# Performance work log

Measured on AMD Instinct MI355X. Metric: run time of the kernel, lower is better.

## Reference

```python
import jax, jax.numpy as jnp
import numpy as np

D_MODEL = 1024
N_HEADS = 16
HEAD_DIM = D_MODEL // N_HEADS
EPS = 1e-5


def _rope_tables(T, dim, dtype):
    inv_freq = 1.0 / (10000.0 ** (np.arange(0, dim, 2, dtype=np.float32) / dim))
    t = np.arange(T, dtype=np.float32)
    freqs = np.einsum('i,j->ij', t, inv_freq)            # [T, dim/2]
    emb = np.concatenate([freqs, freqs], axis=-1)        # [T, dim]
    return jnp.asarray(np.cos(emb), dtype), jnp.asarray(np.sin(emb), dtype)


def _rotate(x, cos, sin):
    # x: [B, T, H, hd]; cos/sin: [T, hd] broadcast over B, H
    c = cos[None, :, None, :]
    s = sin[None, :, None, :]
    x1, x2 = jnp.split(x, 2, axis=-1)
    return x * c + jnp.concatenate([-x2, x1], axis=-1) * s


def setup_inputs() -> dict:
    key = jax.random.key(0)
    k1, k2, k3 = jax.random.split(key, 3)
    B, T = 2, 2048
    x = jax.random.normal(k1, (B, T, D_MODEL), jnp.float32)
    norm_w = jnp.ones((D_MODEL,), jnp.float32)
    w_qkv = jax.random.normal(k2, (D_MODEL, 3 * D_MODEL), jnp.float32) * (D_MODEL ** -0.5)
    w_out = jax.random.normal(k3, (D_MODEL, D_MODEL), jnp.float32) * (D_MODEL ** -0.5)
    return {"x": x, "norm_w": norm_w, "w_qkv": w_qkv, "w_out": w_out}


def reference(x, norm_w, w_qkv, w_out):
    B, T, D = x.shape
    residual = x
    # RMSNorm
    h = x * jax.lax.rsqrt(jnp.mean(x * x, axis=-1, keepdims=True) + EPS) * norm_w
    # QKV projection
    qkv = (h @ w_qkv).reshape(B, T, 3, N_HEADS, HEAD_DIM)
    q, k, v = qkv[:, :, 0], qkv[:, :, 1], qkv[:, :, 2]   # [B, T, H, hd]
    # RoPE
    cos, sin = _rope_tables(T, HEAD_DIM, x.dtype)
    q = _rotate(q, cos, sin)
    k = _rotate(k, cos, sin)
    # Non-causal scaled dot-product attention
    scale = HEAD_DIM ** -0.5
    scores = jnp.einsum('bqhd,bkhd->bhqk', q, k) * scale
    attn = jax.nn.softmax(scores, axis=-1)
    out = jnp.einsum('bhqk,bkhd->bqhd', attn, v).reshape(B, T, D)
    return residual + out @ w_out
```

## Files before the change

kernel.cpp:

```cpp
#include <hip/hip_runtime.h>
#include <hip/hip_bf16.h>

typedef float f32x4 __attribute__((ext_vector_type(4)));
typedef __bf16 bf16x8 __attribute__((ext_vector_type(8)));
typedef __bf16 bf16x4 __attribute__((ext_vector_type(4)));

#define D_MODEL 1024
#define T_SEQ   2048
#define NH      16
#define HD      64

__device__ __forceinline__ void gload16(const void* g, void* l) {
    __builtin_amdgcn_global_load_lds(
        (const __attribute__((address_space(1))) unsigned int*)g,
        (__attribute__((address_space(3))) unsigned int*)l, 16, 0, 0);
}

__global__ __launch_bounds__(256) void k_prep(const float* __restrict__ x,
                                              const float* __restrict__ nw,
                                              const float* __restrict__ w_qkv,
                                              const float* __restrict__ w_out,
                                              __bf16* __restrict__ h,
                                              __bf16* __restrict__ wqkvT,
                                              __bf16* __restrict__ woutT,
                                              float2* __restrict__ tab) {
    __shared__ float tile[32][33];
    __shared__ float red[4];
    const int b = blockIdx.x;
    const int tid = threadIdx.x;

    if (b < 4096) {
        const float* src; __bf16* dst; int R, C, bx, by;
        if (b < 3072) { src = w_qkv; dst = wqkvT; R = 1024; C = 3072; bx = b % 96; by = b / 96; }
        else { int b2 = b - 3072; src = w_out; dst = woutT; R = 1024; C = 1024; bx = b2 % 32; by = b2 / 32; }
        int tx = tid & 31, ty = tid >> 5;
        int c0 = bx * 32, r0 = by * 32;
#pragma unroll
        for (int dy = 0; dy < 32; dy += 8)
            tile[ty + dy][tx] = src[(size_t)(r0 + ty + dy) * C + c0 + tx];
        __syncthreads();
#pragma unroll
        for (int dy = 0; dy < 32; dy += 8)
            dst[(size_t)(c0 + ty + dy) * R + r0 + tx] = (__bf16)tile[tx][ty + dy];
    } else if (b < 8192) {
        int row = b - 4096;
        const float4 v = ((const float4*)(x + (size_t)row * D_MODEL))[tid];
        float ss = v.x * v.x + v.y * v.y + v.z * v.z + v.w * v.w;
#pragma unroll
        for (int off = 32; off > 0; off >>= 1) ss += __shfl_down(ss, off, 64);
        if ((tid & 63) == 0) red[tid >> 6] = ss;
        __syncthreads();
        float total = red[0] + red[1] + red[2] + red[3];
        float rms = rsqrtf(total * (1.f / 1024.f) + 1e-5f);
        const float4 wv = ((const float4*)nw)[tid];
        bf16x4 o;
        o[0] = (__bf16)(v.x * rms * wv.x);
        o[1] = (__bf16)(v.y * rms * wv.y);
        o[2] = (__bf16)(v.z * rms * wv.z);
        o[3] = (__bf16)(v.w * rms * wv.w);
        ((bf16x4*)(h + (size_t)row * D_MODEL))[tid] = o;
    } else {
        int idx = (b - 8192) * 256 + tid;
        int t = idx >> 5, i = idx & 31;
        float inv = __builtin_amdgcn_exp2f(-(float)i * 0.41524101186f);
        float ang = (float)t * inv;
        tab[idx] = make_float2(cosf(ang), sinf(ang));
    }
}

template <int EPI, int BN>
__global__ __launch_bounds__(256) void k_gemm(const __bf16* __restrict__ A,
                                              const __bf16* __restrict__ Bt, int K,
                                              int bxc,
                                              const float2* __restrict__ tab,
                                              __bf16* __restrict__ Qr,
                                              __bf16* __restrict__ Kr,
                                              __bf16* __restrict__ Vt,
                                              const float* __restrict__ resid,
                                              float* __restrict__ outf) {
    constexpr int NF = BN / 32;
    __shared__ __bf16 ldsA[128 * 64];
    __shared__ __bf16 ldsB[BN * 64];
    const int tid  = threadIdx.x;
    const int lane = tid & 63;
    const int wave = tid >> 6;
    const int lin = blockIdx.x;
    const int xcd = lin & 7;
    const int j   = lin >> 3;
    const int bx  = xcd * bxc + j % bxc;
    const int by  = j / bxc;
    const int tile_m = by * 128;
    const int tile_n = bx * BN;
    const int wm = (wave >> 1) * 64;
    const int wn = (wave & 1) * (BN / 2);
    f32x4 acc[4][NF] = {};

    const int srow8 = lane >> 3;
    const int sslot = lane & 7;

    for (int k0 = 0; k0 < K; k0 += 64) {
#pragma unroll
        for (int i = 0; i < 4; i++) {
            int rbase = i * 32 + wave * 8;
            int row = rbase + srow8;
            int scol = (sslot ^ (row & 7)) * 8;
            gload16(A + (size_t)(tile_m + row) * K + k0 + scol,
                    (char*)ldsA + rbase * 128);
        }
#pragma unroll
        for (int i = 0; i < BN / 32; i++) {
            int rbase = i * 32 + wave * 8;
            int row = rbase + srow8;
            int scol = (sslot ^ (row & 7)) * 8;
            gload16(Bt + (size_t)(tile_n + row) * K + k0 + scol,
                    (char*)ldsB + rbase * 128);
        }
        __syncthreads();
#pragma unroll
        for (int kc = 0; kc < 2; kc++) {
            bf16x8 af[4], bfr[NF];
            int s = kc * 4 + (lane >> 4);
#pragma unroll
            for (int mi = 0; mi < 4; mi++) {
                int row = wm + mi * 16 + (lane & 15);
                af[mi] = *(const bf16x8*)((char*)ldsA + row * 128 + ((s ^ (row & 7)) << 4));
            }
#pragma unroll
            for (int nf = 0; nf < NF; nf++) {
                int row = wn + nf * 16 + (lane & 15);
                bfr[nf] = *(const bf16x8*)((char*)ldsB + row * 128 + ((s ^ (row & 7)) << 4));
            }
#pragma unroll
            for (int mi = 0; mi < 4; mi++)
#pragma unroll
                for (int nf = 0; nf < NF; nf++)
                    acc[mi][nf] = __builtin_amdgcn_mfma_f32_16x16x32_bf16(
                        af[mi], bfr[nf], acc[mi][nf], 0, 0, 0);
        }
        __syncthreads();
    }

    if constexpr (EPI == 0) {
        const int nb  = tile_n + wn;
        const int sec = nb >> 10;
        const int hh  = (nb & 1023) >> 6;
        if (sec < 2) {
            __bf16* dstbase = (sec == 0) ? Qr : Kr;
            const float sc = (sec == 0) ? 0.180336880111f : 1.0f;
#pragma unroll
            for (int mi = 0; mi < 4; mi++) {
#pragma unroll
                for (int r = 0; r < 4; r++) {
                    int m = tile_m + wm + mi * 16 + (lane >> 4) * 4 + r;
                    int bb = m >> 11, t = m & 2047;
                    float2 cs0 = tab[t * 32 + (lane & 15)];
                    float2 cs1 = tab[t * 32 + 16 + (lane & 15)];
                    float x0 = acc[mi][0][r], x1 = acc[mi][1][r];
                    float x2 = acc[mi][2][r], x3 = acc[mi][3][r];
                    __bf16* dst = dstbase + ((size_t)(bb * NH + hh) * T_SEQ + t) * HD + (lane & 15);
                    dst[0]  = (__bf16)((x0 * cs0.x - x2 * cs0.y) * sc);
                    dst[16] = (__bf16)((x1 * cs1.x - x3 * cs1.y) * sc);
                    dst[32] = (__bf16)((x2 * cs0.x + x0 * cs0.y) * sc);
                    dst[48] = (__bf16)((x3 * cs1.x + x1 * cs1.y) * sc);
                }
            }
        } else {
#pragma unroll
            for (int mi = 0; mi < 4; mi++) {
                int m0 = tile_m + wm + mi * 16 + (lane >> 4) * 4;
                int bb = m0 >> 11, t0 = m0 & 2047;
#pragma unroll
                for (int nf = 0; nf < 4; nf++) {
                    int d = nf * 16 + (lane & 15);
                    bf16x4 pv;
                    pv[0] = (__bf16)acc[mi][nf][0];
                    pv[1] = (__bf16)acc[mi][nf][1];
                    pv[2] = (__bf16)acc[mi][nf][2];
                    pv[3] = (__bf16)acc[mi][nf][3];
                    *(bf16x4*)(Vt + ((size_t)(bb * NH + hh) * HD + d) * T_SEQ + t0) = pv;
                }
            }
        }
    } else {
#pragma unroll
        for (int mi = 0; mi < 4; mi++)
#pragma unroll
            for (int r = 0; r < 4; r++) {
                int m = tile_m + wm + mi * 16 + (lane >> 4) * 4 + r;
#pragma unroll
                for (int nf = 0; nf < NF; nf++) {
                    int n = tile_n + wn + nf * 16 + (lane & 15);
                    size_t idx = (size_t)m * D_MODEL + n;
                    outf[idx] = resid[idx] + acc[mi][nf][r];
                }
            }
    }
}

__global__ __launch_bounds__(256, 3) void k_attn(const __bf16* __restrict__ Qr,
                                                 const __bf16* __restrict__ Kr,
                                                 const __bf16* __restrict__ Vt,
                                                 __bf16* __restrict__ aout) {
    __shared__ __bf16 ldsK[2][64 * 64];
    __shared__ __bf16 ldsV[2][64 * 64];
    __shared__ __bf16 plds_all[4][32 * 64];
    const int lane = threadIdx.x & 63;
    const int wave = threadIdx.x >> 6;
    const int g  = lane >> 4;
    const int lr = lane & 15;

    const int lin = blockIdx.x;
    const int xcd = lin & 7;
    const int idx = lin >> 3;
    const int bh  = xcd * 4 + (idx >> 4);
    const int qb  = idx & 15;
    const int q0  = qb * 128 + wave * 32;

    const __bf16* Q  = Qr + (size_t)bh * T_SEQ * HD;
    const __bf16* Kp = Kr + (size_t)bh * T_SEQ * HD;
    const __bf16* Vp = Vt + (size_t)bh * HD * T_SEQ;
    char* plds = (char*)plds_all[wave];
    char* Kbase = (char*)&ldsK[0][0];
    char* Vbase = (char*)&ldsV[0][0];

    int kofs[2][4], pwr[4], prd[2];
#pragma unroll
    for (int kc = 0; kc < 2; kc++)
#pragma unroll
        for (int i = 0; i < 4; i++) {
            int row = i * 16 + lr;
            kofs[kc][i] = row * 128 + ((kc * 64 + g * 16) ^ ((row & 7) << 4));
        }
#pragma unroll
    for (int ki = 0; ki < 4; ki++)
        pwr[ki] = lr * 128 + ((ki * 32 + g * 8) ^ ((lr & 7) << 4));
#pragma unroll
    for (int kc = 0; kc < 2; kc++)
        prd[kc] = lr * 128 + ((kc * 64 + g * 16) ^ ((lr & 7) << 4));

    const int srow8 = lane >> 3;
    const int sslot = lane & 7;
    const int scol = (sslot ^ srow8) * 8;
    const int c0 = wave * 2, c1 = wave * 2 + 1;
    const int r0 = c0 * 8 + srow8, r1 = c1 * 8 + srow8;
    const __bf16* kg0 = Kp + (size_t)r0 * HD + scol;
    const __bf16* kg1 = Kp + (size_t)r1 * HD + scol;
    const __bf16* vg0 = Vp + (size_t)r0 * T_SEQ + scol;
    const __bf16* vg1 = Vp + (size_t)r1 * T_SEQ + scol;
    char* Kl0 = Kbase + c0 * 1024;
    char* Kl1 = Kbase + c1 * 1024;
    char* Vl0 = Vbase + c0 * 1024;
    char* Vl1 = Vbase + c1 * 1024;

    bf16x8 qf[2][2];
#pragma unroll
    for (int qi = 0; qi < 2; qi++)
#pragma unroll
        for (int kc = 0; kc < 2; kc++)
            qf[qi][kc] = *(const bf16x8*)(Q + (size_t)(q0 + qi * 16 + lr) * HD +
                                          kc * 32 + g * 8);

    f32x4 o[2][4] = {};
    float mrun[2] = {-1e30f, -1e30f};
    float lrun[2] = {0.f, 0.f};

    gload16(kg0, Kl0); gload16(kg1, Kl1);
    gload16(vg0, Vl0); gload16(vg1, Vl1);
    kg0 += 64 * HD; kg1 += 64 * HD; vg0 += 64; vg1 += 64;
    __syncthreads();

    for (int tile = 0; tile < 32; tile++) {
        const int bufoff = (tile & 1) << 13;
        if (tile < 31) {
            const int nb = bufoff ^ 8192;
            gload16(kg0, Kl0 + nb); gload16(kg1, Kl1 + nb);
            gload16(vg0, Vl0 + nb); gload16(vg1, Vl1 + nb);
            kg0 += 64 * HD; kg1 += 64 * HD; vg0 += 64; vg1 += 64;
        }

        f32x4 s[2][4];
        __builtin_amdgcn_s_setprio(1);
#pragma unroll
        for (int kc = 0; kc < 2; kc++) {
            bf16x8 kf[4];
#pragma unroll
            for (int ki = 0; ki < 4; ki++)
                kf[ki] = *(const bf16x8*)(Kbase + bufoff + kofs[kc][ki]);
#pragma unroll
            for (int qi = 0; qi < 2; qi++)
#pragma unroll
                for (int ki = 0; ki < 4; ki++)
                    s[qi][ki] = (kc == 0)
                        ? __builtin_amdgcn_mfma_f32_16x16x32_bf16(
                              kf[ki], qf[qi][0], f32x4{0.f, 0.f, 0.f, 0.f}, 0, 0, 0)
                        : __builtin_amdgcn_mfma_f32_16x16x32_bf16(
                              kf[ki], qf[qi][1], s[qi][ki], 0, 0, 0);
        }
        __builtin_amdgcn_s_setprio(0);

        float ts2[2];
#pragma unroll
        for (int qi = 0; qi < 2; qi++) {
            float t0 = fmaxf(fmaxf(s[qi][0][0], s[qi][0][1]), fmaxf(s[qi][0][2], s[qi][0][3]));
            float t1 = fmaxf(fmaxf(s[qi][1][0], s[qi][1][1]), fmaxf(s[qi][1][2], s[qi][1][3]));
            float t2 = fmaxf(fmaxf(s[qi][2][0], s[qi][2][1]), fmaxf(s[qi][2][2], s[qi][2][3]));
            float t3 = fmaxf(fmaxf(s[qi][3][0], s[qi][3][1]), fmaxf(s[qi][3][2], s[qi][3][3]));
            float tv = fmaxf(fmaxf(t0, t1), fmaxf(t2, t3));
            tv = fmaxf(tv, __shfl_xor(tv, 16, 64));
            tv = fmaxf(tv, __shfl_xor(tv, 32, 64));
            if (!__all(tv - mrun[qi] <= 8.f)) {
                float mnew = fmaxf(mrun[qi], tv);
                float fac = __builtin_amdgcn_exp2f(mrun[qi] - mnew);
                mrun[qi] = mnew;
                float facT[4];
#pragma unroll
                for (int r = 0; r < 4; r++)
                    facT[r] = __shfl(fac, g * 4 + r, 64);
#pragma unroll
                for (int nf = 0; nf < 4; nf++)
#pragma unroll
                    for (int r = 0; r < 4; r++)
                        o[qi][nf][r] *= facT[r];
                lrun[qi] *= fac;
            }
            float ts = 0.f;
#pragma unroll
            for (int ki = 0; ki < 4; ki++) {
                float p0 = __builtin_amdgcn_exp2f(s[qi][ki][0] - mrun[qi]);
                float p1 = __builtin_amdgcn_exp2f(s[qi][ki][1] - mrun[qi]);
                float p2 = __builtin_amdgcn_exp2f(s[qi][ki][2] - mrun[qi]);
                float p3 = __builtin_amdgcn_exp2f(s[qi][ki][3] - mrun[qi]);
                ts += (p0 + p1) + (p2 + p3);
                bf16x4 pk;
                pk[0] = (__bf16)p0; pk[1] = (__bf16)p1;
                pk[2] = (__bf16)p2; pk[3] = (__bf16)p3;
                *(bf16x4*)(plds + qi * 2048 + pwr[ki]) = pk;
            }
            ts2[qi] = ts;
        }
#pragma unroll
        for (int qi = 0; qi < 2; qi++) {
            float ts = ts2[qi];
            ts += __shfl_xor(ts, 16, 64);
            ts += __shfl_xor(ts, 32, 64);
            lrun[qi] += ts;
        }

        __builtin_amdgcn_s_setprio(1);
#pragma unroll
        for (int kc = 0; kc < 2; kc++) {
            bf16x8 vf[4];
#pragma unroll
            for (int nf = 0; nf < 4; nf++)
                vf[nf] = *(const bf16x8*)(Vbase + bufoff + kofs[kc][nf]);
            bf16x8 pf0 = *(const bf16x8*)(plds + prd[kc]);
            bf16x8 pf1 = *(const bf16x8*)(plds + 2048 + prd[kc]);
#pragma unroll
            for (int nf = 0; nf < 4; nf++)
                o[0][nf] = __builtin_amdgcn_mfma_f32_16x16x32_bf16(pf0, vf[nf], o[0][nf], 0, 0, 0);
#pragma unroll
            for (int nf = 0; nf < 4; nf++)
                o[1][nf] = __builtin_amdgcn_mfma_f32_16x16x32_bf16(pf1, vf[nf], o[1][nf], 0, 0, 0);
        }
        __builtin_amdgcn_s_setprio(0);
        __syncthreads();
    }

    const int bb = bh >> 4, hh = bh & 15;
#pragma unroll
    for (int qi = 0; qi < 2; qi++) {
        float invT[4];
#pragma unroll
        for (int r = 0; r < 4; r++)
            invT[r] = 1.f / __shfl(lrun[qi], g * 4 + r, 64);
#pragma unroll
        for (int r = 0; r < 4; r++) {
            int t = q0 + qi * 16 + g * 4 + r;
#pragma unroll
            for (int nf = 0; nf < 4; nf++) {
                int d = nf * 16 + lr;
                aout[((size_t)(bb * T_SEQ + t)) * D_MODEL + hh * HD + d] =
                    (__bf16)(o[qi][nf][r] * invT[r]);
            }
        }
    }
}

extern "C" void kernel_launch(void* const* d_in, const int* in_sizes, int n_in,
                              void* d_out, int out_size, void* d_ws, size_t ws_size,
                              hipStream_t stream) {
    const float* x      = (const float*)d_in[0];
    const float* norm_w = (const float*)d_in[1];
    const float* w_qkv  = (const float*)d_in[2];
    const float* w_out  = (const float*)d_in[3];
    float* out = (float*)d_out;
    char* ws = (char*)d_ws;

    __bf16* hbuf  = (__bf16*)(ws);
    __bf16* wqkvT = (__bf16*)(ws + ((size_t)8  << 20));
    __bf16* woutT = (__bf16*)(ws + ((size_t)14 << 20));
    float2* tab   = (float2*)(ws + ((size_t)16 << 20));
    __bf16* Qr    = (__bf16*)(ws + ((size_t)17 << 20));
    __bf16* Kr    = (__bf16*)(ws + ((size_t)25 << 20));
    __bf16* Vt    = (__bf16*)(ws + ((size_t)33 << 20));

    k_prep<<<dim3(8448), dim3(256), 0, stream>>>(x, norm_w, w_qkv, w_out,
                                                 hbuf, wqkvT, woutT, tab);
    k_gemm<0, 128><<<dim3(768), dim3(256), 0, stream>>>(hbuf, wqkvT, 1024, 3, tab,
                                                        Qr, Kr, Vt, nullptr, nullptr);
    k_attn<<<dim3(512), dim3(256), 0, stream>>>(Qr, Kr, Vt, hbuf);
    k_gemm<1, 64><<<dim3(512), dim3(256), 0, stream>>>(hbuf, woutT, 1024, 2, nullptr,
                                                       nullptr, nullptr, nullptr, x, out);
}
```

Measured before the change: 205.8 us.

## Double-buffer GEMM LDS tiles and enlarge QKV GEMM tile to 256x256

Generalizes the GEMM kernel over tile and wave shape and adds a two-stage LDS double buffer. The next K-tile's global-to-LDS loads are issued before computing on the current one, with explicit vmcnt waits and raw barriers replacing __syncthreads. The QKV GEMM moves to 256x256 tiles with 512 threads, and the output GEMM uses 128x64 tiles with a plain 2D grid, dropping the XCD-aware block remapping. Larger tiles cut redundant global loads, but they also mean fewer blocks (192 for QKV) and heavier LDS and register use per block.

```diff
diff --git a/kernel.cpp b/kernel.cpp
--- a/kernel.cpp
+++ b/kernel.cpp
@@ -68,76 +68,97 @@
     }
 }
 
-template <int EPI, int BN>
-__global__ __launch_bounds__(256) void k_gemm(const __bf16* __restrict__ A,
-                                              const __bf16* __restrict__ Bt, int K,
-                                              int bxc,
-                                              const float2* __restrict__ tab,
-                                              __bf16* __restrict__ Qr,
-                                              __bf16* __restrict__ Kr,
-                                              __bf16* __restrict__ Vt,
-                                              const float* __restrict__ resid,
-                                              float* __restrict__ outf) {
-    constexpr int NF = BN / 32;
-    __shared__ __bf16 ldsA[128 * 64];
-    __shared__ __bf16 ldsB[BN * 64];
+template <int EPI, int BM, int BN, int WM, int WN, int THREADS, int LB>
+__global__ __launch_bounds__(THREADS, LB)
+void k_gemm(const __bf16* __restrict__ A,
+            const __bf16* __restrict__ Bt, int K,
+            const float2* __restrict__ tab,
+            __bf16* __restrict__ Qr,
+            __bf16* __restrict__ Kr,
+            __bf16* __restrict__ Vt,
+            const float* __restrict__ resid,
+            float* __restrict__ outf) {
+    constexpr int MI = BM / WM / 16;
+    constexpr int NF = BN / WN / 16;
+    constexpr int T8 = THREADS / 8;
+    constexpr int NL = BM / T8 + BN / T8;
+    __shared__ __bf16 ldsA[2 * BM * 64];
+    __shared__ __bf16 ldsB[2 * BN * 64];
     const int tid  = threadIdx.x;
     const int lane = tid & 63;
     const int wave = tid >> 6;
-    const int lin = blockIdx.x;
-    const int xcd = lin & 7;
-    const int j   = lin >> 3;
-    const int bx  = xcd * bxc + j % bxc;
-    const int by  = j / bxc;
-    const int tile_m = by * 128;
-    const int tile_n = bx * BN;
-    const int wm = (wave >> 1) * 64;
-    const int wn = (wave & 1) * (BN / 2);
-    f32x4 acc[4][NF] = {};
-
-    const int srow8 = lane >> 3;
+    const int g    = lane >> 4;
+    const int lr   = lane & 15;
+    const int tile_m = blockIdx.y * BM;
+    const int tile_n = blockIdx.x * BN;
+    const int wm = (wave / WN) * (BM / WM);
+    const int wn = (wave % WN) * (BN / WN);
+    f32x4 acc[MI][NF] = {};
+
+    char* ldsAc = (char*)ldsA;
+    char* ldsBc = (char*)ldsB;
+    const int srow  = lane >> 3;
     const int sslot = lane & 7;
 
-    for (int k0 = 0; k0 < K; k0 += 64) {
-#pragma unroll
-        for (int i = 0; i < 4; i++) {
-            int rbase = i * 32 + wave * 8;
-            int row = rbase + srow8;
-            int scol = (sslot ^ (row & 7)) * 8;
-            gload16(A + (size_t)(tile_m + row) * K + k0 + scol,
-                    (char*)ldsA + rbase * 128);
-        }
-#pragma unroll
-        for (int i = 0; i < BN / 32; i++) {
-            int rbase = i * 32 + wave * 8;
-            int row = rbase + srow8;
-            int scol = (sslot ^ (row & 7)) * 8;
-            gload16(Bt + (size_t)(tile_n + row) * K + k0 + scol,
-                    (char*)ldsB + rbase * 128);
-        }
-        __syncthreads();
+    auto stage = [&](int buf, int k0) {
+#pragma unroll
+        for (int i = 0; i < BM / T8; i++) {
+            int rbase = i * T8 + wave * 8;
+            int row = rbase + srow;
+            int sc = (sslot ^ (row & 7)) * 8;
+            gload16(A + (size_t)(tile_m + row) * K + k0 + sc,
+                    ldsAc + buf * (BM * 128) + rbase * 128);
+        }
+#pragma unroll
+        for (int i = 0; i < BN / T8; i++) {
+            int rbase = i * T8 + wave * 8;
+            int row = rbase + srow;
+            int sc = (sslot ^ (row & 7)) * 8;
+            gload16(Bt + (size_t)(tile_n + row) * K + k0 + sc,
+                    ldsBc + buf * (BN * 128) + rbase * 128);
+        }
+    };
+
+    const int NT = K / 64;
+    stage(0, 0);
+    for (int kt = 0; kt < NT; kt++) {
+        const int cur = kt & 1;
+        if (kt + 1 < NT) {
+            stage(cur ^ 1, (kt + 1) * 64);
+            if constexpr (NL == 8) asm volatile("s_waitcnt vmcnt(8)" ::: "memory");
+            else                   asm volatile("s_waitcnt vmcnt(6)" ::: "memory");
+        } else {
+            asm volatile("s_waitcnt vmcnt(0)" ::: "memory");
+        }
+        __builtin_amdgcn_s_barrier();
+        asm volatile("" ::: "memory");
+
+        const char* Ab = ldsAc + cur * (BM * 128);
+        const char* Bb = ldsBc + cur * (BN * 128);
 #pragma unroll
         for (int kc = 0; kc < 2; kc++) {
-            bf16x8 af[4], bfr[NF];
-            int s = kc * 4 + (lane >> 4);
-#pragma unroll
-            for (int mi = 0; mi < 4; mi++) {
-                int row = wm + mi * 16 + (lane & 15);
-                af[mi] = *(const bf16x8*)((char*)ldsA + row * 128 + ((s ^ (row & 7)) << 4));
+            int s = kc * 4 + g;
+            bf16x8 af[MI], bfr[NF];
+#pragma unroll
+            for (int mi = 0; mi < MI; mi++) {
+                int row = wm + mi * 16 + lr;
+                af[mi] = *(const bf16x8*)(Ab + row * 128 + ((s ^ (row & 7)) << 4));
             }
 #pragma unroll
             for (int nf = 0; nf < NF; nf++) {
-                int row = wn + nf * 16 + (lane & 15);
-                bfr[nf] = *(const bf16x8*)((char*)ldsB + row * 128 + ((s ^ (row & 7)) << 4));
-            }
-#pragma unroll
-            for (int mi = 0; mi < 4; mi++)
+                int row = wn + nf * 16 + lr;
+                bfr[nf] = *(const bf16x8*)(Bb + row * 128 + ((s ^ (row & 7)) << 4));
+            }
+#pragma unroll
+            for (int mi = 0; mi < MI; mi++)
 #pragma unroll
                 for (int nf = 0; nf < NF; nf++)
                     acc[mi][nf] = __builtin_amdgcn_mfma_f32_16x16x32_bf16(
                         af[mi], bfr[nf], acc[mi][nf], 0, 0, 0);
         }
-        __syncthreads();
+        asm volatile("s_waitcnt lgkmcnt(0)" ::: "memory");
+        __builtin_amdgcn_s_barrier();
+        asm volatile("" ::: "memory");
     }
 
     if constexpr (EPI == 0) {
@@ -148,16 +169,16 @@
             __bf16* dstbase = (sec == 0) ? Qr : Kr;
             const float sc = (sec == 0) ? 0.180336880111f : 1.0f;
 #pragma unroll
-            for (int mi = 0; mi < 4; mi++) {
+            for (int mi = 0; mi < MI; mi++) {
 #pragma unroll
                 for (int r = 0; r < 4; r++) {
-                    int m = tile_m + wm + mi * 16 + (lane >> 4) * 4 + r;
+                    int m = tile_m + wm + mi * 16 + g * 4 + r;
                     int bb = m >> 11, t = m & 2047;
-                    float2 cs0 = tab[t * 32 + (lane & 15)];
-                    float2 cs1 = tab[t * 32 + 16 + (lane & 15)];
+                    float2 cs0 = tab[t * 32 + lr];
+                    float2 cs1 = tab[t * 32 + 16 + lr];
                     float x0 = acc[mi][0][r], x1 = acc[mi][1][r];
                     float x2 = acc[mi][2][r], x3 = acc[mi][3][r];
-                    __bf16* dst = dstbase + ((size_t)(bb * NH + hh) * T_SEQ + t) * HD + (lane & 15);
+                    __bf16* dst = dstbase + ((size_t)(bb * NH + hh) * T_SEQ + t) * HD + lr;
                     dst[0]  = (__bf16)((x0 * cs0.x - x2 * cs0.y) * sc);
                     dst[16] = (__bf16)((x1 * cs1.x - x3 * cs1.y) * sc);
                     dst[32] = (__bf16)((x2 * cs0.x + x0 * cs0.y) * sc);
@@ -166,12 +187,12 @@
             }
         } else {
 #pragma unroll
-            for (int mi = 0; mi < 4; mi++) {
-                int m0 = tile_m + wm + mi * 16 + (lane >> 4) * 4;
+            for (int mi = 0; mi < MI; mi++) {
+                int m0 = tile_m + wm + mi * 16 + g * 4;
                 int bb = m0 >> 11, t0 = m0 & 2047;
 #pragma unroll
                 for (int nf = 0; nf < 4; nf++) {
-                    int d = nf * 16 + (lane & 15);
+                    int d = nf * 16 + lr;
                     bf16x4 pv;
                     pv[0] = (__bf16)acc[mi][nf][0];
                     pv[1] = (__bf16)acc[mi][nf][1];
@@ -183,13 +204,13 @@
         }
     } else {
 #pragma unroll
-        for (int mi = 0; mi < 4; mi++)
+        for (int mi = 0; mi < MI; mi++)
 #pragma unroll
             for (int r = 0; r < 4; r++) {
-                int m = tile_m + wm + mi * 16 + (lane >> 4) * 4 + r;
+                int m = tile_m + wm + mi * 16 + g * 4 + r;
 #pragma unroll
                 for (int nf = 0; nf < NF; nf++) {
-                    int n = tile_n + wn + nf * 16 + (lane & 15);
+                    int n = tile_n + wn + nf * 16 + lr;
                     size_t idx = (size_t)m * D_MODEL + n;
                     outf[idx] = resid[idx] + acc[mi][nf][r];
                 }
@@ -406,9 +427,11 @@
 
     k_prep<<<dim3(8448), dim3(256), 0, stream>>>(x, norm_w, w_qkv, w_out,
                                                  hbuf, wqkvT, woutT, tab);
-    k_gemm<0, 128><<<dim3(768), dim3(256), 0, stream>>>(hbuf, wqkvT, 1024, 3, tab,
-                                                        Qr, Kr, Vt, nullptr, nullptr);
+    k_gemm<0, 256, 256, 2, 4, 512, 2>
+        <<<dim3(12, 16), dim3(512), 0, stream>>>(hbuf, wqkvT, 1024, tab,
+                                                 Qr, Kr, Vt, nullptr, nullptr);
     k_attn<<<dim3(512), dim3(256), 0, stream>>>(Qr, Kr, Vt, hbuf);
-    k_gemm<1, 64><<<dim3(512), dim3(256), 0, stream>>>(hbuf, woutT, 1024, 2, nullptr,
-                                                       nullptr, nullptr, nullptr, x, out);
+    k_gemm<1, 128, 64, 2, 2, 256, 4>
+        <<<dim3(16, 32), dim3(256), 0, stream>>>(hbuf, woutT, 1024, nullptr,
+                                                 nullptr, nullptr, nullptr, x, out);
 }
```

Result: no change. 202.1 us (-1.8%).
